# Performance work log

Measured on AMD Instinct MI355X. Metric: run time of the kernel, lower is better.

Reference implementation:

```python
import jax, jax.numpy as jnp
import numpy as np

B, S, D = 2, 2048, 1024
NH, NKV = 16, 4
HD = D // NH          # 64
NREP = NH // NKV      # 4
E, TOPK = 8, 2
CAP_FACTOR = 1.25
HID = 4 * D // 3      # 1365 (hardcoded in MoELayer)
EPS = 1e-6


def rmsnorm(x, w):
    xf = x.astype(jnp.float32)
    y = xf * jax.lax.rsqrt(jnp.mean(xf * xf, axis=-1, keepdims=True) + EPS)
    return y.astype(x.dtype) * w


def apply_rope(x, cos, sin):
    # x: [b, s, h, hd]; cos/sin: [1, s, 1, hd]
    half = x.shape[-1] // 2
    x1, x2 = x[..., :half], x[..., half:]
    ch, sh = cos[..., :half], sin[..., :half]
    return jnp.concatenate([x1 * ch - x2 * sh, x1 * sh + x2 * ch], axis=-1)


def swiglu(x, w1, w2, w3):
    return (jax.nn.silu(x @ w1) * (x @ w3)) @ w2


def setup_inputs():
    key = jax.random.key(0)
    ks = jax.random.split(key, 14)
    x = jax.random.normal(ks[0], (B, S, D), jnp.float32)
    # RoPE tables (standard 10000 base), duplicated halves so cos[..., :half] is valid
    pos = jnp.arange(S, dtype=jnp.float32)[:, None]
    inv = 1.0 / (10000.0 ** (jnp.arange(0, HD, 2, dtype=jnp.float32) / HD))  # [HD/2]
    ang = pos * inv[None, :]                                                # [S, HD/2]
    cos = jnp.concatenate([jnp.cos(ang), jnp.cos(ang)], -1)[None, :, None, :]
    sin = jnp.concatenate([jnp.sin(ang), jnp.sin(ang)], -1)[None, :, None, :]
    # causal additive mask [1,1,S,S]
    causal = jnp.tril(jnp.ones((S, S), bool))
    mask = jnp.where(causal, 0.0, -1e9).astype(jnp.float32)[None, None]
    s = 0.02
    return {
        'x': x, 'cos': cos, 'sin': sin, 'mask': mask,
        'attn_norm_w': jnp.ones((D,), jnp.float32),
        'moe_norm_w': jnp.ones((D,), jnp.float32),
        'wq': jax.random.normal(ks[1], (D, NH * HD), jnp.float32) * s,
        'wk': jax.random.normal(ks[2], (D, NKV * HD), jnp.float32) * s,
        'wv': jax.random.normal(ks[3], (D, NKV * HD), jnp.float32) * s,
        'wo': jax.random.normal(ks[4], (NH * HD, D), jnp.float32) * s,
        'router_w': jax.random.normal(ks[5], (D, E), jnp.float32) * s,
        'ew1': jax.random.normal(ks[6], (E, D, HID), jnp.float32) * s,
        'ew2': jax.random.normal(ks[7], (E, HID, D), jnp.float32) * s,
        'ew3': jax.random.normal(ks[8], (E, D, HID), jnp.float32) * s,
        'sw1': jax.random.normal(ks[9], (D, HID), jnp.float32) * s,
        'sw2': jax.random.normal(ks[10], (HID, D), jnp.float32) * s,
        'sw3': jax.random.normal(ks[11], (D, HID), jnp.float32) * s,
    }


def reference(x, cos, sin, mask, attn_norm_w, moe_norm_w, wq, wk, wv, wo,
              router_w, ew1, ew2, ew3, sw1, sw2, sw3):
    # ---- attention path ----
    xn = rmsnorm(x, attn_norm_w)
    q = (xn @ wq).reshape(B, S, NH, HD)
    k = (xn @ wk).reshape(B, S, NKV, HD)
    v = (xn @ wv).reshape(B, S, NKV, HD)
    q = apply_rope(q, cos, sin)
    k = apply_rope(k, cos, sin)
    new_k, new_v = k, v  # kv cache outputs (no prior cache)
    # repeat_interleave kv heads to NH
    k_rep = jnp.repeat(k, NREP, axis=2)  # [b,s,NH,hd]
    v_rep = jnp.repeat(v, NREP, axis=2)
    scores = jnp.einsum('bqhd,bkhd->bhqk', q, k_rep) / np.sqrt(HD)
    scores = scores + mask[:, :, -S:, :]
    attn = jax.nn.softmax(scores.astype(jnp.float32), axis=-1).astype(q.dtype)
    ao = jnp.einsum('bhqk,bkhd->bqhd', attn, v_rep).reshape(B, S, NH * HD)
    h = x + ao @ wo

    # ---- MoE path ----
    hn = rmsnorm(h, moe_norm_w)
    x_flat = hn.reshape(-1, D)            # [T, D]
    T = x_flat.shape[0]
    logits = x_flat @ router_w            # [T, E]
    probs = jax.nn.softmax(logits, axis=-1)
    w_topk, idx = jax.lax.top_k(probs, TOPK)          # [T, K]
    w_topk = w_topk / jnp.sum(w_topk, axis=-1, keepdims=True)
    onehot = jax.nn.one_hot(idx, E, dtype=jnp.float32)  # [T, K, E]
    counts = jnp.sum(onehot, axis=(0, 1))               # [E]
    util = jnp.mean((counts > 0).astype(jnp.float32)) * 100.0
    fraction = counts / T
    aux_loss = E * jnp.sum(jnp.mean(probs, axis=0) * fraction)
    capacity = int(T * TOPK / E * CAP_FACTOR)
    member = jnp.sum(onehot, axis=1) > 0                 # [T, E] token assigned to expert
    keep = member & (jnp.cumsum(member.astype(jnp.int32), axis=0) <= capacity)
    gate = jnp.sum(w_topk[:, :, None] * onehot, axis=1)  # [T, E] combine weights
    gate = gate * keep.astype(gate.dtype)
    # dense per-expert SwiGLU (same math as masked dispatch; zero-gated tokens vanish)
    h1 = jnp.einsum('td,edh->eth', x_flat, ew1)
    h3 = jnp.einsum('td,edh->eth', x_flat, ew3)
    eo = jnp.einsum('eth,ehd->etd', jax.nn.silu(h1) * h3, ew2)
    moe_out = jnp.einsum('etd,te->td', eo, gate).reshape(B, S, D)
    moe_out = moe_out + swiglu(hn, sw1, sw2, sw3)  # shared expert

    out = h + moe_out
    return out, aux_loss, util, new_k, new_v
```

## Files before the change

kernel.cpp:

```cpp
#include <hip/hip_runtime.h>
#include <hip/hip_bf16.h>
#include <math.h>

typedef __hip_bfloat16 bf16;
typedef __attribute__((ext_vector_type(8))) short short8;
typedef __attribute__((ext_vector_type(4))) float floatx4;

#define SEQ    2048
#define TTOK   4096
#define DM     1024
#define NHEAD  16
#define NKVH   4
#define HD     64
#define NEXP   8
#define HIDDEN 1365
#define HIDP   1408
#define CAPT   1280
#define NSLOT  (NEXP*CAPT)
#define TSLOT  (NSLOT+TTOK)
#define XPE    (CAPT/128)
#define XBT    14

__device__ __forceinline__ void gld16(const void* g, void* l) {
  __builtin_amdgcn_global_load_lds((const __attribute__((address_space(1))) void*)g,
                                   (__attribute__((address_space(3))) void*)l,
                                   16, 0, 0);
}

struct __align__(8) bf4 { bf16 x, y, z, w; };

struct EpiAux {
  const float* cosb; const float* sinb;
  bf16* qb; bf16* kb; bf16* vb; float* newk; float* newv;
};

__global__ __launch_bounds__(256) void transpose_cvt(
    const float* __restrict__ src, bf16* __restrict__ dst,
    int K, int N, int Kp, long srcZ, long dstZ) {
  src += (size_t)blockIdx.z * srcZ;
  dst += (size_t)blockIdx.z * dstZ;
  __shared__ float tile[64][65];
  const int tid = threadIdx.x;
  const int k0 = blockIdx.y * 64, n0 = blockIdx.x * 64;
  const int lr = tid >> 4, lc = (tid & 15) * 4;
#pragma unroll
  for (int i = 0; i < 4; ++i) {
    int k = k0 + lr + i * 16;
    int n = n0 + lc;
    float4 v = {0.f, 0.f, 0.f, 0.f};
    if (k < K) {
      if (n + 3 < N) v = *(const float4*)(src + (size_t)k * N + n);
      else {
        float* vp = (float*)&v;
        for (int e = 0; e < 4; ++e) if (n + e < N) vp[e] = src[(size_t)k * N + n + e];
      }
    }
    tile[lr + i * 16][lc] = v.x; tile[lr + i * 16][lc + 1] = v.y;
    tile[lr + i * 16][lc + 2] = v.z; tile[lr + i * 16][lc + 3] = v.w;
  }
  __syncthreads();
  const int n = tid >> 2, kk0 = (tid & 3) * 16;
  if (n0 + n < N) {
    bf16 buf[16];
#pragma unroll
    for (int e = 0; e < 16; ++e) buf[e] = (bf16)tile[kk0 + e][n];
    bf16* dp = dst + (size_t)(n0 + n) * Kp + k0 + kk0;
    *(short8*)dp = *(short8*)buf;
    *(short8*)(dp + 8) = *(short8*)(buf + 8);
  }
}

__global__ __launch_bounds__(256) void rmsnorm_kernel(
    const float* __restrict__ x, const float* __restrict__ w, bf16* __restrict__ out) {
  int t = blockIdx.x;
  const float* xr = x + (size_t)t * DM;
  float4 xv = *(const float4*)(xr + threadIdx.x * 4);
  float ss = xv.x * xv.x + xv.y * xv.y + xv.z * xv.z + xv.w * xv.w;
#pragma unroll
  for (int off = 1; off < 64; off <<= 1) ss += __shfl_xor(ss, off);
  __shared__ float sred[4];
  if ((threadIdx.x & 63) == 0) sred[threadIdx.x >> 6] = ss;
  __syncthreads();
  float scale = rsqrtf((sred[0] + sred[1] + sred[2] + sred[3]) * (1.f / DM) + 1e-6f);
  float4 wv = *(const float4*)(w + threadIdx.x * 4);
  bf4 o;
  o.x = (bf16)(xv.x * scale * wv.x); o.y = (bf16)(xv.y * scale * wv.y);
  o.z = (bf16)(xv.z * scale * wv.z); o.w = (bf16)(xv.w * scale * wv.w);
  ((bf4*)(out + (size_t)t * DM))[threadIdx.x] = o;
}

__global__ __launch_bounds__(256) void rmsnorm_router_kernel(
    const float* __restrict__ x, const float* __restrict__ w, const float* __restrict__ rw,
    bf16* __restrict__ out, float* __restrict__ probs,
    int* __restrict__ tIdx, float* __restrict__ tW) {
  int t = blockIdx.x;
  int tid = threadIdx.x, lane = tid & 63, wv = tid >> 6;
  const float* xr = x + (size_t)t * DM;
  float4 xv = *(const float4*)(xr + tid * 4);
  float ss = xv.x * xv.x + xv.y * xv.y + xv.z * xv.z + xv.w * xv.w;
#pragma unroll
  for (int off = 1; off < 64; off <<= 1) ss += __shfl_xor(ss, off);
  __shared__ float sred[4];
  __shared__ float red[4][8];
  if (lane == 0) sred[wv] = ss;
// ... 94 lines not shown
  for (int kt = 0; kt < kIters; ++kt) {
    __syncthreads();
#pragma unroll
    for (int it = 0; it < 4; ++it) {
      gld16(aSrc[it], aDst[it]);
      gld16(bSrc[it], bDst[it]);
      aSrc[it] += 64; bSrc[it] += 64;
    }
    __syncthreads();
#pragma unroll
    for (int h = 0; h < 2; ++h) {
      short8 af[4], bfr[4];
#pragma unroll
      for (int i = 0; i < 4; ++i) af[i] = *(const short8*)(As + aOff[i][h]);
#pragma unroll
      for (int j = 0; j < 4; ++j) bfr[j] = *(const short8*)(Bs + bOff[j][h]);
#pragma unroll
      for (int i = 0; i < 4; ++i)
#pragma unroll
        for (int j = 0; j < 4; ++j)
          acc[i][j] = __builtin_amdgcn_mfma_f32_16x16x32_bf16(af[i], bfr[j], acc[i][j], 0, 0, 0);
    }
  }

  if constexpr (EPI == 4) {
#pragma unroll
    for (int i = 0; i < 4; ++i) {
#pragma unroll
      for (int r = 0; r < 4; ++r) {
        int row = wm + i * 16 + quad * 4 + r;
        int t = m0 + row;
        int s = t & (SEQ - 1);
        if (n0 < 1024) {
#pragma unroll
          for (int j = 0; j < 2; ++j) {
            int col = n0 + wn + j * 16 + l15;
            int dlo = col & 63;
            float x1 = acc[i][j][r], x2 = acc[i][j + 2][r];
            float ch = aux.cosb[s * 64 + dlo], sh = aux.sinb[s * 64 + dlo];
            aux.qb[(size_t)t * DM + col]      = (bf16)((x1 * ch - x2 * sh) * 0.125f);
            aux.qb[(size_t)t * DM + col + 32] = (bf16)((x1 * sh + x2 * ch) * 0.125f);
          }
        } else if (n0 < 1280) {
#pragma unroll
          for (int j = 0; j < 2; ++j) {
            int ck = n0 + wn + j * 16 + l15 - 1024;
            int dlo = ck & 63;
            float x1 = acc[i][j][r], x2 = acc[i][j + 2][r];
            float ch = aux.cosb[s * 64 + dlo], sh = aux.sinb[s * 64 + dlo];
            float o1 = x1 * ch - x2 * sh, o2 = x1 * sh + x2 * ch;
            aux.kb[(size_t)t * 256 + ck]        = (bf16)o1;
            aux.kb[(size_t)t * 256 + ck + 32]   = (bf16)o2;
            aux.newk[(size_t)t * 256 + ck]      = o1;
            aux.newk[(size_t)t * 256 + ck + 32] = o2;
          }
        } else {
#pragma unroll
          for (int j = 0; j < 4; ++j) {
            int cv = n0 + wn + j * 16 + l15 - 1280;
            float v = acc[i][j][r];
            aux.vb[(size_t)t * 256 + cv]   = (bf16)v;
            aux.newv[(size_t)t * 256 + cv] = v;
          }
        }
      }
    }
    return;
  }
#pragma unroll
  for (int i = 0; i < 4; ++i) {
#pragma unroll
    for (int j = 0; j < 4; ++j) {
      int col = n0 + wn + j * 16 + l15;
#pragma unroll
      for (int r = 0; r < 4; ++r) {
        int row = wm + i * 16 + quad * 4 + r;
        size_t o = (size_t)(m0 + row) * ldc + col;
        Cf[o] = resid[o] + acc[i][j][r];
      }
    }
  }
}

__device__ __forceinline__ bool slot_block(
    int f, int NY, const int* neCnt, int& expert, int& m0, int& mLimit, int& n0) {
  int xcd = f & 7, lo = f >> 3;
  int xb = lo / NY, y = lo % NY;
  n0 = y * 64;
  if (xb < XPE) {
    expert = xcd;
    int ne = neCnt[xcd];
    if (xb * 128 >= ne) return false;
    m0 = xcd * CAPT + xb * 128;
    mLimit = ne - xb * 128;
    if (mLimit > 128) mLimit = 128;
  } else {
    expert = 8;
    int sb = xcd * 4 + (xb - XPE);
    m0 = NSLOT + sb * 128;
    mLimit = 128;
  }
  return true;
}

__global__ __launch_bounds__(256) void gemm_dual9(
    const bf16* __restrict__ A, const bf16* __restrict__ B1t, const bf16* __restrict__ B3t,
    bf16* __restrict__ mact,
    const int* __restrict__ tokList, const int* __restrict__ neCnt) {
  __shared__ __align__(16) bf16 As[128 * 64];
  __shared__ __align__(16) bf16 B1s[64 * 64];
  __shared__ __align__(16) bf16 B3s[64 * 64];
  const int tid = threadIdx.x, lane = tid & 63, wave = tid >> 6;
  int expert, m0, mLimit, n0;
  if (!slot_block(blockIdx.x, 22, neCnt, expert, m0, mLimit, n0)) return;
  const bf16* B1e = B1t + (long)expert * (HIDDEN * 1024);
  const bf16* B3e = B3t + (long)expert * (HIDDEN * 1024);

  const bf16* aSrc[4]; const bf16* b1Src[2]; const bf16* b3Src[2];
  bf16* aDst[4]; bf16* b1Dst[2]; bf16* b3Dst[2];
#pragma unroll
  for (int it = 0; it < 4; ++it) {
    int c = it * 256 + tid;
    int r = c >> 3, q = c & 7;
    int kq = q ^ (r & 7);
    int rr = r < mLimit ? r : (mLimit - 1);
    aSrc[it] = A + (long)tokList[m0 + rr] * 1024 + kq * 8;
    aDst[it] = As + (size_t)(it * 256 + wave * 64) * 8;
  }
#pragma unroll
  for (int it = 0; it < 2; ++it) {
    int c = it * 256 + tid;
    int r = c >> 3, q = c & 7;
    int kq = q ^ (r & 7);
    int nn = n0 + r; if (nn > HIDDEN - 1) nn = HIDDEN - 1;
    b1Src[it] = B1e + (long)nn * 1024 + kq * 8;
    b3Src[it] = B3e + (long)nn * 1024 + kq * 8;
    b1Dst[it] = B1s + (size_t)(it * 256 + wave * 64) * 8;
    b3Dst[it] = B3s + (size_t)(it * 256 + wave * 64) * 8;
  }

  floatx4 acc1[4][2], acc3[4][2];
#pragma unroll
  for (int i = 0; i < 4; ++i)
#pragma unroll
    for (int j = 0; j < 2; ++j) {
      floatx4 z = {0.f, 0.f, 0.f, 0.f};
      acc1[i][j] = z; acc3[i][j] = z;
    }

  const int wm = (wave & 1) * 64, wn = (wave >> 1) * 32;
  const int l15 = lane & 15, quad = lane >> 4;
  int aOff[4][2], bOff[2][2];
#pragma unroll
  for (int h = 0; h < 2; ++h) {
#pragma unroll
    for (int i = 0; i < 4; ++i) {
      int m = wm + i * 16 + l15;
      aOff[i][h] = (((m << 3) | ((h * 4 + quad) ^ (m & 7))) << 3);
    }
#pragma unroll
    for (int j = 0; j < 2; ++j) {
      int n = wn + j * 16 + l15;
      bOff[j][h] = (((n << 3) | ((h * 4 + quad) ^ (n & 7))) << 3);
    }
  }

  for (int kt = 0; kt < 16; ++kt) {
    __syncthreads();
#pragma unroll
    for (int it = 0; it < 4; ++it) { gld16(aSrc[it], aDst[it]); aSrc[it] += 64; }
#pragma unroll
    for (int it = 0; it < 2; ++it) {
      gld16(b1Src[it], b1Dst[it]); b1Src[it] += 64;
      gld16(b3Src[it], b3Dst[it]); b3Src[it] += 64;
    }
    __syncthreads();
#pragma unroll
    for (int h = 0; h < 2; ++h) {
      short8 af[4];
#pragma unroll
      for (int i = 0; i < 4; ++i) af[i] = *(const short8*)(As + aOff[i][h]);
#pragma unroll
      for (int j = 0; j < 2; ++j) {
        short8 b1f = *(const short8*)(B1s + bOff[j][h]);
        short8 b3f = *(const short8*)(B3s + bOff[j][h]);
#pragma unroll
        for (int i = 0; i < 4; ++i) {
          acc1[i][j] = __builtin_amdgcn_mfma_f32_16x16x32_bf16(af[i], b1f, acc1[i][j], 0, 0, 0);
          acc3[i][j] = __builtin_amdgcn_mfma_f32_16x16x32_bf16(af[i], b3f, acc3[i][j], 0, 0, 0);
        }
      }
    }
  }

#pragma unroll
  for (int i = 0; i < 4; ++i) {
#pragma unroll
    for (int j = 0; j < 2; ++j) {
      int col = n0 + wn + j * 16 + l15;
#pragma unroll
      for (int r = 0; r < 4; ++r) {
        int row = wm + i * 16 + quad * 4 + r;
        if (row >= mLimit) continue;
        float a1 = acc1[i][j][r], a3 = acc3[i][j][r];
        float sl = a1 / (1.f + __expf(-a1));
        mact[(size_t)(m0 + row) * HIDP + col] = (col < HIDDEN) ? (bf16)(sl * a3) : (bf16)0.f;
      }
    }
  }
}

__global__ __launch_bounds__(256) void gemm_down9(
    const bf16* __restrict__ A, const bf16* __restrict__ B2t,
    bf16* __restrict__ eo,
    const float* __restrict__ gateW, const int* __restrict__ neCnt) {
  __shared__ __align__(16) bf16 As[128 * 64];
  __shared__ __align__(16) bf16 Bs[64 * 64];
  const int tid = threadIdx.x, lane = tid & 63, wave = tid >> 6;
  int expert, m0, mLimit, n0;
  if (!slot_block(blockIdx.x, 16, neCnt, expert, m0, mLimit, n0)) return;
  const bf16* Be = B2t + (long)expert * (1024 * HIDP);

  const bf16* aSrc[4]; const bf16* bSrc[2];
  bf16* aDst[4]; bf16* bDst[2];
#pragma unroll
  for (int it = 0; it < 4; ++it) {
    int c = it * 256 + tid;
    int r = c >> 3, q = c & 7;
    int kq = q ^ (r & 7);
    int rr = r < mLimit ? r : (mLimit - 1);
    aSrc[it] = A + (long)(m0 + rr) * HIDP + kq * 8;
    aDst[it] = As + (size_t)(it * 256 + wave * 64) * 8;
  }
#pragma unroll
  for (int it = 0; it < 2; ++it) {
    int c = it * 256 + tid;
    int r = c >> 3, q = c & 7;
    int kq = q ^ (r & 7);
    bSrc[it] = Be + (long)(n0 + r) * HIDP + kq * 8;
    bDst[it] = Bs + (size_t)(it * 256 + wave * 64) * 8;
  }

  floatx4 acc[4][2];
#pragma unroll
  for (int i = 0; i < 4; ++i)
#pragma unroll
    for (int j = 0; j < 2; ++j) { floatx4 z = {0.f, 0.f, 0.f, 0.f}; acc[i][j] = z; }

  const int wm = (wave & 1) * 64, wn = (wave >> 1) * 32;
  const int l15 = lane & 15, quad = lane >> 4;
  int aOff[4][2], bOff[2][2];
#pragma unroll
  for (int h = 0; h < 2; ++h) {
#pragma unroll
    for (int i = 0; i < 4; ++i) {
      int m = wm + i * 16 + l15;
      aOff[i][h] = (((m << 3) | ((h * 4 + quad) ^ (m & 7))) << 3);
    }
#pragma unroll
    for (int j = 0; j < 2; ++j) {
      int n = wn + j * 16 + l15;
      bOff[j][h] = (((n << 3) | ((h * 4 + quad) ^ (n & 7))) << 3);
    }
  }

  for (int kt = 0; kt < 22; ++kt) {
    __syncthreads();
#pragma unroll
    for (int it = 0; it < 4; ++it) { gld16(aSrc[it], aDst[it]); aSrc[it] += 64; }
#pragma unroll
    for (int it = 0; it < 2; ++it) { gld16(bSrc[it], bDst[it]); bSrc[it] += 64; }
    __syncthreads();
#pragma unroll
    for (int h = 0; h < 2; ++h) {
      short8 af[4];
#pragma unroll
      for (int i = 0; i < 4; ++i) af[i] = *(const short8*)(As + aOff[i][h]);
#pragma unroll
      for (int j = 0; j < 2; ++j) {
        short8 bf = *(const short8*)(Bs + bOff[j][h]);
#pragma unroll
        for (int i = 0; i < 4; ++i)
          acc[i][j] = __builtin_amdgcn_mfma_f32_16x16x32_bf16(af[i], bf, acc[i][j], 0, 0, 0);
      }
    }
  }

#pragma unroll
  for (int i = 0; i < 4; ++i) {
#pragma unroll
    for (int j = 0; j < 2; ++j) {
      int col = n0 + wn + j * 16 + l15;
#pragma unroll
      for (int r = 0; r < 4; ++r) {
        int row = wm + i * 16 + quad * 4 + r;
        if (row >= mLimit) continue;
        eo[(size_t)(m0 + row) * 1024 + col] = (bf16)(gateW[m0 + row] * acc[i][j][r]);
      }
    }
  }
}

__global__ __launch_bounds__(256) void vt_kernel(
    const bf16* __restrict__ vb, bf16* __restrict__ vt) {
  __shared__ __align__(16) bf16 tile[64 * 72];
  int t0 = blockIdx.x * 64, bg = blockIdx.y;
  int b = bg >> 2, g = bg & 3;
  int tid = threadIdx.x;
  for (int c = tid; c < 512; c += 256) {
    int r = c >> 3, d8 = (c & 7) * 8;
    *(short8*)(tile + r * 72 + d8) =
        *(const short8*)(vb + (size_t)(b * SEQ + t0 + r) * 256 + g * 64 + d8);
  }
  __syncthreads();
  for (int c = tid; c < 512; c += 256) {
    int d = c >> 3, s8 = (c & 7) * 8;
    bf16 tmp[8];
#pragma unroll
    for (int x = 0; x < 8; ++x) tmp[x] = tile[(s8 + x) * 72 + d];
    *(short8*)(vt + ((size_t)bg * 64 + d) * SEQ + t0 + s8) = *(short8*)tmp;
  }
}

__global__ __launch_bounds__(256) void attn_kernel(
    const bf16* __restrict__ Q, const bf16* __restrict__ Kc, const bf16* __restrict__ Vt,
    bf16* __restrict__ AO) {
  __shared__ __align__(16) bf16 Qs[64 * 64];
  __shared__ __align__(16) bf16 Ks[64 * 64];
  __shared__ __align__(16) bf16 Vs[64 * 64];
  __shared__ __align__(16) bf16 Ps[4][16 * 64];
  const int pairI = blockIdx.x, h = blockIdx.y, b = blockIdx.z;
  const int g = h >> 2;
  const int tid = threadIdx.x, lane = tid & 63, wave = tid >> 6;
  const int l15 = lane & 15, quad = lane >> 4;

  const bf16* kSrc[2]; const bf16* vSrc[2]; bf16* kDst[2]; bf16* vDst[2];
#pragma unroll
  for (int it = 0; it < 2; ++it) {
    int c = it * 256 + tid;
    int r = c >> 3, p = c & 7;
    int kq = p ^ (r & 7);
    kSrc[it] = Kc + (size_t)(b * SEQ + r) * 256 + g * 64 + kq * 8;
    vSrc[it] = Vt + ((size_t)(b * 4 + g) * 64 + r) * SEQ + kq * 8;
    kDst[it] = Ks + (size_t)(it * 256 + wave * 64) * 8;
    vDst[it] = Vs + (size_t)(it * 256 + wave * 64) * 8;
  }

  int qOff[2], kvOff[4][2], pOff[2];
#pragma unroll
  for (int hh = 0; hh < 2; ++hh) {
    int m = wave * 16 + l15;
    qOff[hh] = (m << 6) + (((hh * 4 + quad) ^ (m & 7)) << 3);
#pragma unroll
    for (int j = 0; j < 4; ++j) {
      int n = j * 16 + l15;
      kvOff[j][hh] = (n << 6) + (((hh * 4 + quad) ^ (n & 7)) << 3);
    }
    int cblk = (hh * 2 + (quad >> 1)) ^ (l15 >> 2);
    pOff[hh] = (l15 << 6) + (cblk << 4) + ((quad & 1) << 3);
  }
  bf16* pw = &Ps[wave][0];
  const int rowl = wave * 16 + quad * 4;

  short8 onesb;
#pragma unroll
  for (int e = 0; e < 8; ++e) onesb[e] = (short)0x3F80;

  for (int ph = 0; ph < 2; ++ph) {
    const int q0 = (ph == 0 ? pairI : 31 - pairI) * 64;
    __syncthreads();
#pragma unroll
    for (int it = 0; it < 2; ++it) {
      int c = it * 256 + tid;
      int r = c >> 3, p = c & 7;
      int kq = p ^ (r & 7);
      gld16(Q + (size_t)(b * SEQ + q0 + r) * DM + h * 64 + kq * 8,
            Qs + (size_t)(it * 256 + wave * 64) * 8);
    }
// ... 164 lines not shown
  const float* cosb  = (const float*)d_in[1];
  const float* sinb  = (const float*)d_in[2];
  const float* attnw = (const float*)d_in[4];
  const float* moew  = (const float*)d_in[5];
  const float* wq  = (const float*)d_in[6];
  const float* wk  = (const float*)d_in[7];
  const float* wv  = (const float*)d_in[8];
  const float* wo  = (const float*)d_in[9];
  const float* rw  = (const float*)d_in[10];
  const float* ew1 = (const float*)d_in[11];
  const float* ew2 = (const float*)d_in[12];
  const float* ew3 = (const float*)d_in[13];
  const float* sw1 = (const float*)d_in[14];
  const float* sw2 = (const float*)d_in[15];
  const float* sw3 = (const float*)d_in[16];

  float* outp = (float*)d_out;
  float* auxp = outp + 4194304;
  float* newk = outp + 4194306;
  float* newv = newk + 1048576;

  char* wsp = (char*)d_ws;
  size_t off = 0;
  auto alloc = [&](size_t bytes) -> void* {
    void* p = wsp + off; off += (bytes + 255) & ~(size_t)255; return p;
  };
  bf16* wqkvT = (bf16*)alloc((size_t)1536 * 1024 * 2);
  bf16* woT   = (bf16*)alloc((size_t)1024 * 1024 * 2);
  bf16* ew1T  = (bf16*)alloc((size_t)9 * HIDDEN * 1024 * 2);
  bf16* ew3T  = (bf16*)alloc((size_t)9 * HIDDEN * 1024 * 2);
  bf16* ew2T  = (bf16*)alloc((size_t)9 * 1024 * HIDP * 2);
  bf16* xn    = (bf16*)alloc((size_t)TTOK * DM * 2);
  bf16* qb    = (bf16*)alloc((size_t)TTOK * DM * 2);
  bf16* kb    = (bf16*)alloc((size_t)TTOK * 256 * 2);
  bf16* vb    = (bf16*)alloc((size_t)TTOK * 256 * 2);
  bf16* vt    = (bf16*)alloc((size_t)TTOK * 256 * 2);
  bf16* ao    = (bf16*)alloc((size_t)TTOK * DM * 2);
  float* hbuf = (float*)alloc((size_t)TTOK * DM * 4);
  bf16* hn    = (bf16*)alloc((size_t)TTOK * DM * 2);
  float* probs = (float*)alloc((size_t)TTOK * 8 * 4);
  int*   tIdx  = (int*)alloc((size_t)TTOK * 2 * 4);
  float* tW    = (float*)alloc((size_t)TTOK * 2 * 4);
  int*   tokList = (int*)alloc((size_t)TSLOT * 4);
  float* gateW   = (float*)alloc((size_t)TSLOT * 4);
  int*   neCnt   = (int*)alloc(64);
  int*   cntFull = (int*)alloc(64);
  int*   slotOf  = (int*)alloc((size_t)TTOK * 2 * 4);
  bf16*  mact = (bf16*)alloc((size_t)TSLOT * HIDP * 2);
  bf16*  eo   = (bf16*)alloc((size_t)TSLOT * DM * 2);

  EpiAux nil{};
  EpiAux ropeAux{cosb, sinb, qb, kb, vb, newk, newv};

  transpose_cvt<<<dim3(16, 16, 1), 256, 0, stream>>>(wq, wqkvT, 1024, 1024, 1024, 0, 0);
  transpose_cvt<<<dim3(4, 16, 1), 256, 0, stream>>>(wk, wqkvT + (size_t)1024 * 1024, 1024, 256, 1024, 0, 0);
  transpose_cvt<<<dim3(4, 16, 1), 256, 0, stream>>>(wv, wqkvT + (size_t)1280 * 1024, 1024, 256, 1024, 0, 0);
  transpose_cvt<<<dim3(16, 16, 1), 256, 0, stream>>>(wo, woT, 1024, 1024, 1024, 0, 0);
  transpose_cvt<<<dim3(22, 16, NEXP), 256, 0, stream>>>(ew1, ew1T, 1024, HIDDEN, 1024,
      (long)1024 * HIDDEN, (long)HIDDEN * 1024);
  transpose_cvt<<<dim3(22, 16, NEXP), 256, 0, stream>>>(ew3, ew3T, 1024, HIDDEN, 1024,
      (long)1024 * HIDDEN, (long)HIDDEN * 1024);
  transpose_cvt<<<dim3(16, 22, NEXP), 256, 0, stream>>>(ew2, ew2T, HIDDEN, 1024, HIDP,
      (long)HIDDEN * 1024, (long)1024 * HIDP);
  transpose_cvt<<<dim3(22, 16, 1), 256, 0, stream>>>(sw1, ew1T + (size_t)8 * HIDDEN * 1024,
      1024, HIDDEN, 1024, 0, 0);
  transpose_cvt<<<dim3(22, 16, 1), 256, 0, stream>>>(sw3, ew3T + (size_t)8 * HIDDEN * 1024,
      1024, HIDDEN, 1024, 0, 0);
  transpose_cvt<<<dim3(16, 22, 1), 256, 0, stream>>>(sw2, ew2T + (size_t)8 * 1024 * HIDP,
      HIDDEN, 1024, HIDP, 0, 0);

  rmsnorm_kernel<<<TTOK, 256, 0, stream>>>(x, attnw, xn);
  gemm_bt<4><<<8 * 4 * 12, 256, 0, stream>>>(
      xn, wqkvT, TTOK, 1536, 1024, 1024, 1024, 4, nullptr, 0, nullptr, ropeAux);
  vt_kernel<<<dim3(32, 8), 256, 0, stream>>>(vb, vt);
  attn_kernel<<<dim3(16, NHEAD, 2), 256, 0, stream>>>(qb, kb, vt, ao);
  gemm_bt<2><<<8 * 4 * 8, 256, 0, stream>>>(
      ao, woT, TTOK, 1024, 1024, 1024, 1024, 4, hbuf, 1024, x, nil);

  rmsnorm_router_kernel<<<TTOK, 256, 0, stream>>>(hbuf, moew, rw, hn, probs, tIdx, tW);
  hipMemsetAsync(slotOf, 0xFF, (size_t)TTOK * 2 * 4, stream);
  assign_kernel<<<9, 256, 0, stream>>>(tIdx, tW, tokList, gateW, neCnt, cntFull, slotOf);
  aux_kernel<<<1, 256, 0, stream>>>(probs, cntFull, auxp);

  gemm_dual9<<<8 * XBT * 22, 256, 0, stream>>>(hn, ew1T, ew3T, mact, tokList, neCnt);
  gemm_down9<<<8 * XBT * 16, 256, 0, stream>>>(mact, ew2T, eo, gateW, neCnt);
  combine_kernel<<<TTOK, 256, 0, stream>>>(outp, hbuf, eo, slotOf);
}
```

Baseline: 583.2 us.

## Enlarge MoE GEMM tiles to 256x128 with double-buffered LDS prefetch

Both expert GEMMs (the fused gate/up SwiGLU GEMM and the down projection) move from 128x64 tiles with 256 threads to 256x128 tiles with 512 threads. Each of the 8 waves now computes a 128x32 sub-tile. The single-buffered load/sync loop is replaced by a two-stage LDS pipeline that prefetches k-tile kt+2 while computing kt, with explicit vmcnt waits, barriers and MFMA priority hints. The aim is more operand reuse per global load and hiding of load latency. In exchange, LDS use reaches about 128KB per block in the dual kernel, which limits occupancy to one block per CU, and the grid becomes much smaller.

```diff
diff --git a/kernel.cpp b/kernel.cpp
--- a/kernel.cpp
+++ b/kernel.cpp
@@ -18,8 +18,8 @@
 #define CAPT   1280
 #define NSLOT  (NEXP*CAPT)
 #define TSLOT  (NSLOT+TTOK)
-#define XPE    (CAPT/128)
-#define XBT    14
+#define XPE2   (CAPT/256)
+#define XBT2   7
 
 __device__ __forceinline__ void gld16(const void* g, void* l) {
   __builtin_amdgcn_global_load_lds((const __attribute__((address_space(1))) void*)g,
@@ -280,37 +280,37 @@
   }
 }
 
-__device__ __forceinline__ bool slot_block(
+__device__ __forceinline__ bool slot_block256(
     int f, int NY, const int* neCnt, int& expert, int& m0, int& mLimit, int& n0) {
   int xcd = f & 7, lo = f >> 3;
   int xb = lo / NY, y = lo % NY;
-  n0 = y * 64;
-  if (xb < XPE) {
+  n0 = y * 128;
+  if (xb < XPE2) {
     expert = xcd;
     int ne = neCnt[xcd];
-    if (xb * 128 >= ne) return false;
-    m0 = xcd * CAPT + xb * 128;
-    mLimit = ne - xb * 128;
-    if (mLimit > 128) mLimit = 128;
+    if (xb * 256 >= ne) return false;
+    m0 = xcd * CAPT + xb * 256;
+    mLimit = ne - xb * 256;
+    if (mLimit > 256) mLimit = 256;
   } else {
     expert = 8;
-    int sb = xcd * 4 + (xb - XPE);
-    m0 = NSLOT + sb * 128;
-    mLimit = 128;
+    int sb = xcd * 2 + (xb - XPE2);
+    m0 = NSLOT + sb * 256;
+    mLimit = 256;
   }
   return true;
 }
 
-__global__ __launch_bounds__(256) void gemm_dual9(
+__global__ __launch_bounds__(512, 2) void gemm_dual9(
     const bf16* __restrict__ A, const bf16* __restrict__ B1t, const bf16* __restrict__ B3t,
     bf16* __restrict__ mact,
     const int* __restrict__ tokList, const int* __restrict__ neCnt) {
-  __shared__ __align__(16) bf16 As[128 * 64];
-  __shared__ __align__(16) bf16 B1s[64 * 64];
-  __shared__ __align__(16) bf16 B3s[64 * 64];
+  __shared__ __align__(16) bf16 As[2][256 * 64];
+  __shared__ __align__(16) bf16 B1s[2][128 * 64];
+  __shared__ __align__(16) bf16 B3s[2][128 * 64];
   const int tid = threadIdx.x, lane = tid & 63, wave = tid >> 6;
   int expert, m0, mLimit, n0;
-  if (!slot_block(blockIdx.x, 22, neCnt, expert, m0, mLimit, n0)) return;
+  if (!slot_block256(blockIdx.x, 11, neCnt, expert, m0, mLimit, n0)) return;
   const bf16* B1e = B1t + (long)expert * (HIDDEN * 1024);
   const bf16* B3e = B3t + (long)expert * (HIDDEN * 1024);
 
@@ -318,87 +318,139 @@
   bf16* aDst[4]; bf16* b1Dst[2]; bf16* b3Dst[2];
 #pragma unroll
   for (int it = 0; it < 4; ++it) {
-    int c = it * 256 + tid;
+    int c = it * 512 + tid;
     int r = c >> 3, q = c & 7;
     int kq = q ^ (r & 7);
     int rr = r < mLimit ? r : (mLimit - 1);
     aSrc[it] = A + (long)tokList[m0 + rr] * 1024 + kq * 8;
-    aDst[it] = As + (size_t)(it * 256 + wave * 64) * 8;
+    aDst[it] = &As[0][0] + (size_t)(it * 512 + wave * 64) * 8;
   }
 #pragma unroll
   for (int it = 0; it < 2; ++it) {
-    int c = it * 256 + tid;
+    int c = it * 512 + tid;
     int r = c >> 3, q = c & 7;
     int kq = q ^ (r & 7);
     int nn = n0 + r; if (nn > HIDDEN - 1) nn = HIDDEN - 1;
     b1Src[it] = B1e + (long)nn * 1024 + kq * 8;
     b3Src[it] = B3e + (long)nn * 1024 + kq * 8;
-    b1Dst[it] = B1s + (size_t)(it * 256 + wave * 64) * 8;
-    b3Dst[it] = B3s + (size_t)(it * 256 + wave * 64) * 8;
-  }
-
-  floatx4 acc1[4][2], acc3[4][2];
-#pragma unroll
-  for (int i = 0; i < 4; ++i)
+    b1Dst[it] = &B1s[0][0] + (size_t)(it * 512 + wave * 64) * 8;
+    b3Dst[it] = &B3s[0][0] + (size_t)(it * 512 + wave * 64) * 8;
+  }
+
+  auto stage = [&](int buf, int ktile) {
+    const long ko = (long)ktile * 64;
+    const size_t sa = (size_t)buf * (256 * 64);
+    const size_t sb = (size_t)buf * (128 * 64);
+#pragma unroll
+    for (int it = 0; it < 4; ++it) gld16(aSrc[it] + ko, aDst[it] + sa);
+#pragma unroll
+    for (int it = 0; it < 2; ++it) {
+      gld16(b1Src[it] + ko, b1Dst[it] + sb);
+      gld16(b3Src[it] + ko, b3Dst[it] + sb);
+    }
+  };
+
+  floatx4 acc1[8][2], acc3[8][2];
+#pragma unroll
+  for (int i = 0; i < 8; ++i)
 #pragma unroll
     for (int j = 0; j < 2; ++j) {
       floatx4 z = {0.f, 0.f, 0.f, 0.f};
       acc1[i][j] = z; acc3[i][j] = z;
     }
 
-  const int wm = (wave & 1) * 64, wn = (wave >> 1) * 32;
+  const int wr = wave & 1, wc = wave >> 1;
   const int l15 = lane & 15, quad = lane >> 4;
-  int aOff[4][2], bOff[2][2];
+  int aOff[8][2], bOff[2][2];
 #pragma unroll
   for (int h = 0; h < 2; ++h) {
 #pragma unroll
-    for (int i = 0; i < 4; ++i) {
-      int m = wm + i * 16 + l15;
-      aOff[i][h] = (((m << 3) | ((h * 4 + quad) ^ (m & 7))) << 3);
+    for (int i = 0; i < 8; ++i) {
+      int m = wr * 128 + i * 16 + l15;
+      aOff[i][h] = (m << 6) + (((h * 4 + quad) ^ (m & 7)) << 3);
     }
 #pragma unroll
     for (int j = 0; j < 2; ++j) {
-      int n = wn + j * 16 + l15;
-      bOff[j][h] = (((n << 3) | ((h * 4 + quad) ^ (n & 7))) << 3);
-    }
-  }
+      int n = wc * 32 + j * 16 + l15;
+      bOff[j][h] = (n << 6) + (((h * 4 + quad) ^ (n & 7)) << 3);
+    }
+  }
+
+  stage(0, 0);
+  stage(1, 1);
+  asm volatile("s_waitcnt vmcnt(8)" ::: "memory");
+  __builtin_amdgcn_s_barrier();
 
   for (int kt = 0; kt < 16; ++kt) {
-    __syncthreads();
-#pragma unroll
-    for (int it = 0; it < 4; ++it) { gld16(aSrc[it], aDst[it]); aSrc[it] += 64; }
-#pragma unroll
-    for (int it = 0; it < 2; ++it) {
-      gld16(b1Src[it], b1Dst[it]); b1Src[it] += 64;
-      gld16(b3Src[it], b3Dst[it]); b3Src[it] += 64;
-    }
-    __syncthreads();
-#pragma unroll
-    for (int h = 0; h < 2; ++h) {
-      short8 af[4];
-#pragma unroll
-      for (int i = 0; i < 4; ++i) af[i] = *(const short8*)(As + aOff[i][h]);
-#pragma unroll
-      for (int j = 0; j < 2; ++j) {
-        short8 b1f = *(const short8*)(B1s + bOff[j][h]);
-        short8 b3f = *(const short8*)(B3s + bOff[j][h]);
-#pragma unroll
-        for (int i = 0; i < 4; ++i) {
-          acc1[i][j] = __builtin_amdgcn_mfma_f32_16x16x32_bf16(af[i], b1f, acc1[i][j], 0, 0, 0);
-          acc3[i][j] = __builtin_amdgcn_mfma_f32_16x16x32_bf16(af[i], b3f, acc3[i][j], 0, 0, 0);
-        }
-      }
-    }
-  }
-
-#pragma unroll
-  for (int i = 0; i < 4; ++i) {
+    const bf16* Ab  = &As[0][0]  + (size_t)(kt & 1) * (256 * 64);
+    const bf16* B1b = &B1s[0][0] + (size_t)(kt & 1) * (128 * 64);
+    const bf16* B3b = &B3s[0][0] + (size_t)(kt & 1) * (128 * 64);
+#pragma unroll
+    for (int mh = 0; mh < 2; ++mh) {
+      short8 af[4][2];
+#pragma unroll
+      for (int i = 0; i < 4; ++i)
+#pragma unroll
+        for (int h = 0; h < 2; ++h)
+          af[i][h] = *(const short8*)(Ab + aOff[mh * 4 + i][h]);
+      {
+        short8 b1f[2][2];
+#pragma unroll
+        for (int j = 0; j < 2; ++j)
+#pragma unroll
+          for (int h = 0; h < 2; ++h)
+            b1f[j][h] = *(const short8*)(B1b + bOff[j][h]);
+        __builtin_amdgcn_s_setprio(1);
+#pragma unroll
+        for (int h = 0; h < 2; ++h)
+#pragma unroll
+          for (int j = 0; j < 2; ++j)
+#pragma unroll
+            for (int i = 0; i < 4; ++i)
+              acc1[mh * 4 + i][j] = __builtin_amdgcn_mfma_f32_16x16x32_bf16(
+                  af[i][h], b1f[j][h], acc1[mh * 4 + i][j], 0, 0, 0);
+        __builtin_amdgcn_s_setprio(0);
+      }
+      __builtin_amdgcn_s_barrier();
+      {
+        short8 b3f[2][2];
+#pragma unroll
+        for (int j = 0; j < 2; ++j)
+#pragma unroll
+          for (int h = 0; h < 2; ++h)
+            b3f[j][h] = *(const short8*)(B3b + bOff[j][h]);
+        __builtin_amdgcn_s_setprio(1);
+#pragma unroll
+        for (int h = 0; h < 2; ++h)
+#pragma unroll
+          for (int j = 0; j < 2; ++j)
+#pragma unroll
+            for (int i = 0; i < 4; ++i)
+              acc3[mh * 4 + i][j] = __builtin_amdgcn_mfma_f32_16x16x32_bf16(
+                  af[i][h], b3f[j][h], acc3[mh * 4 + i][j], 0, 0, 0);
+        __builtin_amdgcn_s_setprio(0);
+      }
+      __builtin_amdgcn_s_barrier();
+    }
+    asm volatile("s_waitcnt lgkmcnt(0)" ::: "memory");
+    __builtin_amdgcn_s_barrier();
+    if (kt < 14) {
+      stage(kt & 1, kt + 2);
+      asm volatile("s_waitcnt vmcnt(8)" ::: "memory");
+    } else {
+      asm volatile("s_waitcnt vmcnt(0)" ::: "memory");
+    }
+    __builtin_amdgcn_s_barrier();
+  }
+
+#pragma unroll
+  for (int i = 0; i < 8; ++i) {
 #pragma unroll
     for (int j = 0; j < 2; ++j) {
-      int col = n0 + wn + j * 16 + l15;
+      int col = n0 + wc * 32 + j * 16 + l15;
 #pragma unroll
       for (int r = 0; r < 4; ++r) {
-        int row = wm + i * 16 + quad * 4 + r;
+        int row = wr * 128 + i * 16 + quad * 4 + r;
         if (row >= mLimit) continue;
         float a1 = acc1[i][j][r], a3 = acc3[i][j][r];
         float sl = a1 / (1.f + __expf(-a1));
@@ -408,90 +460,123 @@
   }
 }
 
-__global__ __launch_bounds__(256) void gemm_down9(
+__global__ __launch_bounds__(512, 2) void gemm_down9(
     const bf16* __restrict__ A, const bf16* __restrict__ B2t,
     bf16* __restrict__ eo,
     const float* __restrict__ gateW, const int* __restrict__ neCnt) {
-  __shared__ __align__(16) bf16 As[128 * 64];
-  __shared__ __align__(16) bf16 Bs[64 * 64];
+  __shared__ __align__(16) bf16 As[2][256 * 64];
+  __shared__ __align__(16) bf16 Bs[2][128 * 64];
   const int tid = threadIdx.x, lane = tid & 63, wave = tid >> 6;
   int expert, m0, mLimit, n0;
-  if (!slot_block(blockIdx.x, 16, neCnt, expert, m0, mLimit, n0)) return;
+  if (!slot_block256(blockIdx.x, 8, neCnt, expert, m0, mLimit, n0)) return;
   const bf16* Be = B2t + (long)expert * (1024 * HIDP);
 
   const bf16* aSrc[4]; const bf16* bSrc[2];
   bf16* aDst[4]; bf16* bDst[2];
 #pragma unroll
   for (int it = 0; it < 4; ++it) {
-    int c = it * 256 + tid;
+    int c = it * 512 + tid;
     int r = c >> 3, q = c & 7;
     int kq = q ^ (r & 7);
     int rr = r < mLimit ? r : (mLimit - 1);
     aSrc[it] = A + (long)(m0 + rr) * HIDP + kq * 8;
-    aDst[it] = As + (size_t)(it * 256 + wave * 64) * 8;
+    aDst[it] = &As[0][0] + (size_t)(it * 512 + wave * 64) * 8;
   }
 #pragma unroll
   for (int it = 0; it < 2; ++it) {
-    int c = it * 256 + tid;
+    int c = it * 512 + tid;
     int r = c >> 3, q = c & 7;
     int kq = q ^ (r & 7);
     bSrc[it] = Be + (long)(n0 + r) * HIDP + kq * 8;
-    bDst[it] = Bs + (size_t)(it * 256 + wave * 64) * 8;
-  }
-
-  floatx4 acc[4][2];
-#pragma unroll
-  for (int i = 0; i < 4; ++i)
+    bDst[it] = &Bs[0][0] + (size_t)(it * 512 + wave * 64) * 8;
+  }
+
+  auto stage = [&](int buf, int ktile) {
+    const long ko = (long)ktile * 64;
+    const size_t sa = (size_t)buf * (256 * 64);
+    const size_t sb = (size_t)buf * (128 * 64);
+#pragma unroll
+    for (int it = 0; it < 4; ++it) gld16(aSrc[it] + ko, aDst[it] + sa);
+#pragma unroll
+    for (int it = 0; it < 2; ++it) gld16(bSrc[it] + ko, bDst[it] + sb);
+  };
+
+  floatx4 acc[8][2];
+#pragma unroll
+  for (int i = 0; i < 8; ++i)
 #pragma unroll
     for (int j = 0; j < 2; ++j) { floatx4 z = {0.f, 0.f, 0.f, 0.f}; acc[i][j] = z; }
 
-  const int wm = (wave & 1) * 64, wn = (wave >> 1) * 32;
+  const int wr = wave & 1, wc = wave >> 1;
   const int l15 = lane & 15, quad = lane >> 4;
-  int aOff[4][2], bOff[2][2];
+  int aOff[8][2], bOff[2][2];
 #pragma unroll
   for (int h = 0; h < 2; ++h) {
 #pragma unroll
-    for (int i = 0; i < 4; ++i) {
-      int m = wm + i * 16 + l15;
-      aOff[i][h] = (((m << 3) | ((h * 4 + quad) ^ (m & 7))) << 3);
+    for (int i = 0; i < 8; ++i) {
+      int m = wr * 128 + i * 16 + l15;
+      aOff[i][h] = (m << 6) + (((h * 4 + quad) ^ (m & 7)) << 3);
     }
 #pragma unroll
     for (int j = 0; j < 2; ++j) {
-      int n = wn + j * 16 + l15;
-      bOff[j][h] = (((n << 3) | ((h * 4 + quad) ^ (n & 7))) << 3);
-    }
-  }
+      int n = wc * 32 + j * 16 + l15;
+      bOff[j][h] = (n << 6) + (((h * 4 + quad) ^ (n & 7)) << 3);
+    }
+  }
+
+  stage(0, 0);
+  stage(1, 1);
+  asm volatile("s_waitcnt vmcnt(6)" ::: "memory");
+  __builtin_amdgcn_s_barrier();
 
   for (int kt = 0; kt < 22; ++kt) {
-    __syncthreads();
-#pragma unroll
-    for (int it = 0; it < 4; ++it) { gld16(aSrc[it], aDst[it]); aSrc[it] += 64; }
-#pragma unroll
-    for (int it = 0; it < 2; ++it) { gld16(bSrc[it], bDst[it]); bSrc[it] += 64; }
-    __syncthreads();
-#pragma unroll
-    for (int h = 0; h < 2; ++h) {
-      short8 af[4];
-#pragma unroll
-      for (int i = 0; i < 4; ++i) af[i] = *(const short8*)(As + aOff[i][h]);
-#pragma unroll
-      for (int j = 0; j < 2; ++j) {
-        short8 bf = *(const short8*)(Bs + bOff[j][h]);
-#pragma unroll
-        for (int i = 0; i < 4; ++i)
-          acc[i][j] = __builtin_amdgcn_mfma_f32_16x16x32_bf16(af[i], bf, acc[i][j], 0, 0, 0);
-      }
-    }
-  }
-
-#pragma unroll
-  for (int i = 0; i < 4; ++i) {
+    const bf16* Ab = &As[0][0] + (size_t)(kt & 1) * (256 * 64);
+    const bf16* Bb = &Bs[0][0] + (size_t)(kt & 1) * (128 * 64);
+#pragma unroll
+    for (int mh = 0; mh < 2; ++mh) {
+      short8 af[4][2];
+#pragma unroll
+      for (int i = 0; i < 4; ++i)
+#pragma unroll
+        for (int h = 0; h < 2; ++h)
+          af[i][h] = *(const short8*)(Ab + aOff[mh * 4 + i][h]);
+      short8 bf[2][2];
+#pragma unroll
+      for (int j = 0; j < 2; ++j)
+#pragma unroll
+        for (int h = 0; h < 2; ++h)
+          bf[j][h] = *(const short8*)(Bb + bOff[j][h]);
+      __builtin_amdgcn_s_setprio(1);
+#pragma unroll
+      for (int h = 0; h < 2; ++h)
+#pragma unroll
+        for (int j = 0; j < 2; ++j)
+#pragma unroll
+          for (int i = 0; i < 4; ++i)
+            acc[mh * 4 + i][j] = __builtin_amdgcn_mfma_f32_16x16x32_bf16(
+                af[i][h], bf[j][h], acc[mh * 4 + i][j], 0, 0, 0);
+      __builtin_amdgcn_s_setprio(0);
+      __builtin_amdgcn_s_barrier();
+    }
+    asm volatile("s_waitcnt lgkmcnt(0)" ::: "memory");
+    __builtin_amdgcn_s_barrier();
+    if (kt < 20) {
+      stage(kt & 1, kt + 2);
+      asm volatile("s_waitcnt vmcnt(6)" ::: "memory");
+    } else {
+      asm volatile("s_waitcnt vmcnt(0)" ::: "memory");
+    }
+    __builtin_amdgcn_s_barrier();
+  }
+
+#pragma unroll
+  for (int i = 0; i < 8; ++i) {
 #pragma unroll
     for (int j = 0; j < 2; ++j) {
-      int col = n0 + wn + j * 16 + l15;
+      int col = n0 + wc * 32 + j * 16 + l15;
 #pragma unroll
       for (int r = 0; r < 4; ++r) {
-        int row = wm + i * 16 + quad * 4 + r;
+        int row = wr * 128 + i * 16 + quad * 4 + r;
         if (row >= mLimit) continue;
         eo[(size_t)(m0 + row) * 1024 + col] = (bf16)(gateW[m0 + row] * acc[i][j][r]);
       }
@@ -822,7 +907,7 @@
   assign_kernel<<<9, 256, 0, stream>>>(tIdx, tW, tokList, gateW, neCnt, cntFull, slotOf);
   aux_kernel<<<1, 256, 0, stream>>>(probs, cntFull, auxp);
 
-  gemm_dual9<<<8 * XBT * 22, 256, 0, stream>>>(hn, ew1T, ew3T, mact, tokList, neCnt);
-  gemm_down9<<<8 * XBT * 16, 256, 0, stream>>>(mact, ew2T, eo, gateW, neCnt);
+  gemm_dual9<<<8 * XBT2 * 11, 512, 0, stream>>>(hn, ew1T, ew3T, mact, tokList, neCnt);
+  gemm_down9<<<8 * XBT2 * 8, 512, 0, stream>>>(mact, ew2T, eo, gateW, neCnt);
   combine_kernel<<<TTOK, 256, 0, stream>>>(outp, hbuf, eo, slotOf);
 }
```

Measured after the change: 632.9 us. 8.5% more time.

## Enlarge MoE gate/up GEMM tile to 256x128 with double-buffered LDS pipeline

Applied to the files above, without the earlier changes.

The fused W1/W3 expert GEMM now uses 512-thread blocks with a 256x128 output tile instead of 128x64, and the slot-to-block mapping is redone for 256-row tiles. The K loop is double-buffered: loads for the next K tile are issued in quarters between the MFMA phases, fenced with explicit vmcnt/lgkmcnt waits, barriers and s_setprio. The aim is more reuse per loaded tile and hiding global-to-LDS latency behind matrix math. In exchange each block uses 128KB of LDS, runs fewer blocks, wastes more on partially filled expert tiles, and relies on hand-counted waitcnt values that could break if the load order changes.

```diff
diff --git a/kernel.cpp b/kernel.cpp
--- a/kernel.cpp
+++ b/kernel.cpp
@@ -20,6 +20,8 @@
 #define TSLOT  (NSLOT+TTOK)
 #define XPE    (CAPT/128)
 #define XBT    14
+#define XPE2   (CAPT/256)
+#define XBT2   7
 
 __device__ __forceinline__ void gld16(const void* g, void* l) {
   __builtin_amdgcn_global_load_lds((const __attribute__((address_space(1))) void*)g,
@@ -301,16 +303,37 @@
   return true;
 }
 
-__global__ __launch_bounds__(256) void gemm_dual9(
+__device__ __forceinline__ bool slot_block256(
+    int f, int NY, const int* neCnt, int& expert, int& m0, int& mLimit, int& n0) {
+  int xcd = f & 7, lo = f >> 3;
+  int xb = lo / NY, y = lo % NY;
+  n0 = y * 128;
+  if (xb < XPE2) {
+    expert = xcd;
+    int ne = neCnt[xcd];
+    if (xb * 256 >= ne) return false;
+    m0 = xcd * CAPT + xb * 256;
+    mLimit = ne - xb * 256;
+    if (mLimit > 256) mLimit = 256;
+  } else {
+    expert = 8;
+    int sb = xcd * 2 + (xb - XPE2);
+    m0 = NSLOT + sb * 256;
+    mLimit = 256;
+  }
+  return true;
+}
+
+__global__ __launch_bounds__(512, 2) void gemm_dual9(
     const bf16* __restrict__ A, const bf16* __restrict__ B1t, const bf16* __restrict__ B3t,
     bf16* __restrict__ mact,
     const int* __restrict__ tokList, const int* __restrict__ neCnt) {
-  __shared__ __align__(16) bf16 As[128 * 64];
-  __shared__ __align__(16) bf16 B1s[64 * 64];
-  __shared__ __align__(16) bf16 B3s[64 * 64];
+  __shared__ __align__(16) bf16 As[2][256 * 64];
+  __shared__ __align__(16) bf16 B1s[2][128 * 64];
+  __shared__ __align__(16) bf16 B3s[2][128 * 64];
   const int tid = threadIdx.x, lane = tid & 63, wave = tid >> 6;
   int expert, m0, mLimit, n0;
-  if (!slot_block(blockIdx.x, 22, neCnt, expert, m0, mLimit, n0)) return;
+  if (!slot_block256(blockIdx.x, 11, neCnt, expert, m0, mLimit, n0)) return;
   const bf16* B1e = B1t + (long)expert * (HIDDEN * 1024);
   const bf16* B3e = B3t + (long)expert * (HIDDEN * 1024);
 
@@ -318,87 +341,178 @@
   bf16* aDst[4]; bf16* b1Dst[2]; bf16* b3Dst[2];
 #pragma unroll
   for (int it = 0; it < 4; ++it) {
-    int c = it * 256 + tid;
+    int c = it * 512 + tid;
     int r = c >> 3, q = c & 7;
     int kq = q ^ (r & 7);
     int rr = r < mLimit ? r : (mLimit - 1);
     aSrc[it] = A + (long)tokList[m0 + rr] * 1024 + kq * 8;
-    aDst[it] = As + (size_t)(it * 256 + wave * 64) * 8;
+    aDst[it] = &As[0][0] + (size_t)(it * 512 + wave * 64) * 8;
   }
 #pragma unroll
   for (int it = 0; it < 2; ++it) {
-    int c = it * 256 + tid;
+    int c = it * 512 + tid;
     int r = c >> 3, q = c & 7;
     int kq = q ^ (r & 7);
     int nn = n0 + r; if (nn > HIDDEN - 1) nn = HIDDEN - 1;
     b1Src[it] = B1e + (long)nn * 1024 + kq * 8;
     b3Src[it] = B3e + (long)nn * 1024 + kq * 8;
-    b1Dst[it] = B1s + (size_t)(it * 256 + wave * 64) * 8;
-    b3Dst[it] = B3s + (size_t)(it * 256 + wave * 64) * 8;
-  }
-
-  floatx4 acc1[4][2], acc3[4][2];
-#pragma unroll
-  for (int i = 0; i < 4; ++i)
+    b1Dst[it] = &B1s[0][0] + (size_t)(it * 512 + wave * 64) * 8;
+    b3Dst[it] = &B3s[0][0] + (size_t)(it * 512 + wave * 64) * 8;
+  }
+
+  floatx4 acc1[8][2], acc3[8][2];
+#pragma unroll
+  for (int i = 0; i < 8; ++i)
 #pragma unroll
     for (int j = 0; j < 2; ++j) {
       floatx4 z = {0.f, 0.f, 0.f, 0.f};
       acc1[i][j] = z; acc3[i][j] = z;
     }
 
-  const int wm = (wave & 1) * 64, wn = (wave >> 1) * 32;
+  const int wr = wave & 1, wc = wave >> 1;
   const int l15 = lane & 15, quad = lane >> 4;
-  int aOff[4][2], bOff[2][2];
+  int aOff[8][2], bOff[2][2];
 #pragma unroll
   for (int h = 0; h < 2; ++h) {
 #pragma unroll
-    for (int i = 0; i < 4; ++i) {
-      int m = wm + i * 16 + l15;
-      aOff[i][h] = (((m << 3) | ((h * 4 + quad) ^ (m & 7))) << 3);
+    for (int i = 0; i < 8; ++i) {
+      int m = wr * 128 + i * 16 + l15;
+      aOff[i][h] = (m << 6) + (((h * 4 + quad) ^ (m & 7)) << 3);
     }
 #pragma unroll
     for (int j = 0; j < 2; ++j) {
-      int n = wn + j * 16 + l15;
-      bOff[j][h] = (((n << 3) | ((h * 4 + quad) ^ (n & 7))) << 3);
-    }
-  }
+      int n = wc * 32 + j * 16 + l15;
+      bOff[j][h] = (n << 6) + (((h * 4 + quad) ^ (n & 7)) << 3);
+    }
+  }
+
+  {
+#pragma unroll
+    for (int it = 0; it < 4; ++it) gld16(aSrc[it], aDst[it]);
+#pragma unroll
+    for (int it = 0; it < 2; ++it) gld16(b1Src[it], b1Dst[it]);
+#pragma unroll
+    for (int it = 0; it < 2; ++it) gld16(b3Src[it], b3Dst[it]);
+  }
+  asm volatile("s_waitcnt vmcnt(2)" ::: "memory");
+  __builtin_amdgcn_s_barrier();
 
   for (int kt = 0; kt < 16; ++kt) {
-    __syncthreads();
-#pragma unroll
-    for (int it = 0; it < 4; ++it) { gld16(aSrc[it], aDst[it]); aSrc[it] += 64; }
-#pragma unroll
-    for (int it = 0; it < 2; ++it) {
-      gld16(b1Src[it], b1Dst[it]); b1Src[it] += 64;
-      gld16(b3Src[it], b3Dst[it]); b3Src[it] += 64;
-    }
-    __syncthreads();
-#pragma unroll
-    for (int h = 0; h < 2; ++h) {
-      short8 af[4];
-#pragma unroll
-      for (int i = 0; i < 4; ++i) af[i] = *(const short8*)(As + aOff[i][h]);
-#pragma unroll
-      for (int j = 0; j < 2; ++j) {
-        short8 b1f = *(const short8*)(B1s + bOff[j][h]);
-        short8 b3f = *(const short8*)(B3s + bOff[j][h]);
-#pragma unroll
-        for (int i = 0; i < 4; ++i) {
-          acc1[i][j] = __builtin_amdgcn_mfma_f32_16x16x32_bf16(af[i], b1f, acc1[i][j], 0, 0, 0);
-          acc3[i][j] = __builtin_amdgcn_mfma_f32_16x16x32_bf16(af[i], b3f, acc3[i][j], 0, 0, 0);
-        }
-      }
-    }
-  }
-
-#pragma unroll
-  for (int i = 0; i < 4; ++i) {
+    const int cur = kt & 1, nxt = cur ^ 1;
+    const bf16* Ab  = &As[0][0]  + (size_t)cur * (256 * 64);
+    const bf16* B1b = &B1s[0][0] + (size_t)cur * (128 * 64);
+    const bf16* B3b = &B3s[0][0] + (size_t)cur * (128 * 64);
+    const bool pf = (kt < 15);
+    const long ko1 = (long)(kt + 1) * 64;
+    const size_t sa = (size_t)nxt * (256 * 64);
+    const size_t sb = (size_t)nxt * (128 * 64);
+
+    short8 bb[2][2];
+    {
+      short8 a0[4][2];
+#pragma unroll
+      for (int i = 0; i < 4; ++i)
+#pragma unroll
+        for (int h = 0; h < 2; ++h) a0[i][h] = *(const short8*)(Ab + aOff[i][h]);
+#pragma unroll
+      for (int j = 0; j < 2; ++j)
+#pragma unroll
+        for (int h = 0; h < 2; ++h) bb[j][h] = *(const short8*)(B1b + bOff[j][h]);
+      if (pf) { gld16(aSrc[0] + ko1, aDst[0] + sa); gld16(aSrc[1] + ko1, aDst[1] + sa); }
+      __builtin_amdgcn_s_barrier();
+      asm volatile("s_waitcnt lgkmcnt(0)" ::: "memory");
+      __builtin_amdgcn_s_setprio(1);
+#pragma unroll
+      for (int h = 0; h < 2; ++h)
+#pragma unroll
+        for (int j = 0; j < 2; ++j)
+#pragma unroll
+          for (int i = 0; i < 4; ++i)
+            acc1[i][j] = __builtin_amdgcn_mfma_f32_16x16x32_bf16(
+                a0[i][h], bb[j][h], acc1[i][j], 0, 0, 0);
+      __builtin_amdgcn_s_setprio(0);
+      __builtin_amdgcn_s_barrier();
+    }
+    {
+      short8 a1[4][2];
+#pragma unroll
+      for (int i = 0; i < 4; ++i)
+#pragma unroll
+        for (int h = 0; h < 2; ++h) a1[i][h] = *(const short8*)(Ab + aOff[4 + i][h]);
+      if (pf) { gld16(aSrc[2] + ko1, aDst[2] + sa); gld16(aSrc[3] + ko1, aDst[3] + sa); }
+      __builtin_amdgcn_s_barrier();
+      asm volatile("s_waitcnt lgkmcnt(0)" ::: "memory");
+      __builtin_amdgcn_s_setprio(1);
+#pragma unroll
+      for (int h = 0; h < 2; ++h)
+#pragma unroll
+        for (int j = 0; j < 2; ++j)
+#pragma unroll
+          for (int i = 0; i < 4; ++i)
+            acc1[4 + i][j] = __builtin_amdgcn_mfma_f32_16x16x32_bf16(
+                a1[i][h], bb[j][h], acc1[4 + i][j], 0, 0, 0);
+      __builtin_amdgcn_s_setprio(0);
+      if (pf) asm volatile("s_waitcnt vmcnt(4)" ::: "memory");
+      else    asm volatile("s_waitcnt vmcnt(0)" ::: "memory");
+      __builtin_amdgcn_s_barrier();
+    }
+    {
+      short8 a0[4][2];
+#pragma unroll
+      for (int i = 0; i < 4; ++i)
+#pragma unroll
+        for (int h = 0; h < 2; ++h) a0[i][h] = *(const short8*)(Ab + aOff[i][h]);
+#pragma unroll
+      for (int j = 0; j < 2; ++j)
+#pragma unroll
+        for (int h = 0; h < 2; ++h) bb[j][h] = *(const short8*)(B3b + bOff[j][h]);
+      if (pf) { gld16(b1Src[0] + ko1, b1Dst[0] + sb); gld16(b1Src[1] + ko1, b1Dst[1] + sb); }
+      __builtin_amdgcn_s_barrier();
+      asm volatile("s_waitcnt lgkmcnt(0)" ::: "memory");
+      __builtin_amdgcn_s_setprio(1);
+#pragma unroll
+      for (int h = 0; h < 2; ++h)
+#pragma unroll
+        for (int j = 0; j < 2; ++j)
+#pragma unroll
+          for (int i = 0; i < 4; ++i)
+            acc3[i][j] = __builtin_amdgcn_mfma_f32_16x16x32_bf16(
+                a0[i][h], bb[j][h], acc3[i][j], 0, 0, 0);
+      __builtin_amdgcn_s_setprio(0);
+      __builtin_amdgcn_s_barrier();
+    }
+    {
+      short8 a1[4][2];
+#pragma unroll
+      for (int i = 0; i < 4; ++i)
+#pragma unroll
+        for (int h = 0; h < 2; ++h) a1[i][h] = *(const short8*)(Ab + aOff[4 + i][h]);
+      if (pf) { gld16(b3Src[0] + ko1, b3Dst[0] + sb); gld16(b3Src[1] + ko1, b3Dst[1] + sb); }
+      __builtin_amdgcn_s_barrier();
+      asm volatile("s_waitcnt lgkmcnt(0)" ::: "memory");
+      __builtin_amdgcn_s_setprio(1);
+#pragma unroll
+      for (int h = 0; h < 2; ++h)
+#pragma unroll
+        for (int j = 0; j < 2; ++j)
+#pragma unroll
+          for (int i = 0; i < 4; ++i)
+            acc3[4 + i][j] = __builtin_amdgcn_mfma_f32_16x16x32_bf16(
+                a1[i][h], bb[j][h], acc3[4 + i][j], 0, 0, 0);
+      __builtin_amdgcn_s_setprio(0);
+      if (pf) asm volatile("s_waitcnt vmcnt(2)" ::: "memory");
+      __builtin_amdgcn_s_barrier();
+    }
+  }
+
+#pragma unroll
+  for (int i = 0; i < 8; ++i) {
 #pragma unroll
     for (int j = 0; j < 2; ++j) {
-      int col = n0 + wn + j * 16 + l15;
+      int col = n0 + wc * 32 + j * 16 + l15;
 #pragma unroll
       for (int r = 0; r < 4; ++r) {
-        int row = wm + i * 16 + quad * 4 + r;
+        int row = wr * 128 + i * 16 + quad * 4 + r;
         if (row >= mLimit) continue;
         float a1 = acc1[i][j][r], a3 = acc3[i][j][r];
         float sl = a1 / (1.f + __expf(-a1));
@@ -822,7 +936,7 @@
   assign_kernel<<<9, 256, 0, stream>>>(tIdx, tW, tokList, gateW, neCnt, cntFull, slotOf);
   aux_kernel<<<1, 256, 0, stream>>>(probs, cntFull, auxp);
 
-  gemm_dual9<<<8 * XBT * 22, 256, 0, stream>>>(hn, ew1T, ew3T, mact, tokList, neCnt);
+  gemm_dual9<<<8 * XBT2 * 11, 512, 0, stream>>>(hn, ew1T, ew3T, mact, tokList, neCnt);
   gemm_down9<<<8 * XBT * 16, 256, 0, stream>>>(mact, ew2T, eo, gateW, neCnt);
   combine_kernel<<<TTOK, 256, 0, stream>>>(outp, hbuf, eo, slotOf);
 }
```

After: 602.7 us. 1.03x slower.
